# Optimization experiments

Measured on AMD Instinct MI355X. Metric: run time of the kernel, lower is better.

## Reference

```python
import jax, jax.numpy as jnp
import numpy as np

NH, NKV, HD = 32, 8, 64
ROPE_BASE = 10000.0


def _rope_tables(L, hd):
    inv_freq = 1.0 / (ROPE_BASE ** (jnp.arange(0, hd, 2, dtype=jnp.float32) / hd))
    t = jnp.arange(L, dtype=jnp.float32)
    freqs = jnp.outer(t, inv_freq)              # (L, hd/2)
    emb = jnp.concatenate([freqs, freqs], -1)   # (L, hd)
    return jnp.cos(emb), jnp.sin(emb)


def _rotate_half(x):
    h = x.shape[-1] // 2
    return jnp.concatenate([-x[..., h:], x[..., :h]], axis=-1)


def _apply_rope(x, cos, sin):
    # x: (B, H, L, hd); cos/sin: (L, hd) broadcast over B, H
    return x * cos[None, None] + _rotate_half(x) * sin[None, None]


def setup_inputs() -> dict:
    key = jax.random.key(0)
    ks = jax.random.split(key, 5)
    B, L, H = 2, 2048, 2048
    s = 0.02
    return {
        "x": jax.random.normal(ks[0], (B, L, H), dtype=jnp.float32),
        "wq": jax.random.normal(ks[1], (NH * HD, H), dtype=jnp.float32) * s,
        "wk": jax.random.normal(ks[2], (NKV * HD, H), dtype=jnp.float32) * s,
        "wv": jax.random.normal(ks[3], (NKV * HD, H), dtype=jnp.float32) * s,
        "wo": jax.random.normal(ks[4], (H, NH * HD), dtype=jnp.float32) * s,
    }


def reference(x, wq, wk, wv, wo):
    B, L, H = x.shape
    rep = NH // NKV
    q = (x @ wq.T).reshape(B, L, NH, HD).transpose(0, 2, 1, 3)    # (B, nh, L, hd)
    k = (x @ wk.T).reshape(B, L, NKV, HD).transpose(0, 2, 1, 3)   # (B, nkv, L, hd)
    v = (x @ wv.T).reshape(B, L, NKV, HD).transpose(0, 2, 1, 3)
    cos, sin = _rope_tables(L, HD)
    q = _apply_rope(q, cos, sin)
    k = _apply_rope(k, cos, sin)
    # GQA: group q heads instead of repeating K/V (same math as repeat_interleave)
    qg = q.reshape(B, NKV, rep, L, HD)
    scores = jnp.einsum("bgrqd,bgkd->bgrqk", qg, k) / jnp.sqrt(jnp.float32(HD))
    causal = jnp.tril(jnp.ones((L, L), dtype=bool))
    scores = jnp.where(causal, scores, jnp.float32(-jnp.inf))
    probs = jax.nn.softmax(scores, axis=-1)
    out = jnp.einsum("bgrqk,bgkd->bgrqd", probs, v)               # (B, nkv, rep, L, hd)
    out = out.reshape(B, NH, L, HD).transpose(0, 2, 1, 3).reshape(B, L, NH * HD)
    return out @ wo.T
```

## Files before the change

### kernel.cpp

```cpp
#include <hip/hip_runtime.h>

using u16 = unsigned short;
using u32 = unsigned int;
typedef __attribute__((ext_vector_type(8))) short bf16x8;
typedef __attribute__((ext_vector_type(4))) float f32x4;
typedef __attribute__((ext_vector_type(4))) float float4v;
typedef __attribute__((ext_vector_type(4))) unsigned short us4;
typedef __attribute__((ext_vector_type(2))) unsigned int u32x2;

__device__ __forceinline__ u16 f2bf(float f) {
  union { float f; unsigned u; } v; v.f = f;
  unsigned r = v.u + 0x7fffu + ((v.u >> 16) & 1u);
  return (u16)(r >> 16);
}

__device__ __forceinline__ u32 cvtpk(float a, float b) {
  u32 r;
  asm("v_cvt_pk_bf16_f32 %0, %1, %2" : "=v"(r) : "v"(a), "v"(b));
  return r;
}

__device__ __forceinline__ void glds16(const void* g, void* l) {
  __builtin_amdgcn_global_load_lds(
      (const __attribute__((address_space(1))) void*)g,
      (__attribute__((address_space(3))) void*)l, 16, 0, 0);
}

__device__ __forceinline__ void lgkm0() {
  asm volatile("s_waitcnt lgkmcnt(0)" ::: "memory");
}

#define MFMA(a, b, c) __builtin_amdgcn_mfma_f32_16x16x32_bf16((a), (b), (c), 0, 0, 0)

#define QSCALE 0.1803368801111601f

__global__ __launch_bounds__(256) void cvt_all(
    const float* __restrict__ x, const float* __restrict__ wq,
    const float* __restrict__ wk, const float* __restrict__ wv,
    const float* __restrict__ wo, u16* __restrict__ x_bf,
    u16* __restrict__ wqkv, u16* __restrict__ wo_bf) {
  int i = blockIdx.x * 256 + threadIdx.x;
  const float4v* src;
  us4* dst;
  if (i < 2097152) {
    src = (const float4v*)x + i; dst = (us4*)x_bf + i;
  } else if (i < 3145728) {
    int j = i - 2097152; src = (const float4v*)wq + j; dst = (us4*)wqkv + j;
  } else if (i < 3407872) {
    int j = i - 3145728; src = (const float4v*)wk + j; dst = (us4*)wqkv + 1048576 + j;
  } else if (i < 3670016) {
    int j = i - 3407872; src = (const float4v*)wv + j; dst = (us4*)wqkv + 1310720 + j;
  } else {
    int j = i - 3670016; src = (const float4v*)wo + j; dst = (us4*)wo_bf + j;
  }
  float4v v = *src;
  us4 o;
  o[0] = f2bf(v[0]); o[1] = f2bf(v[1]); o[2] = f2bf(v[2]); o[3] = f2bf(v[3]);
  *dst = o;
}

__global__ __launch_bounds__(256) void rope_cs(float2* __restrict__ cs) {
  int i = blockIdx.x * 256 + threadIdx.x;
  if (i >= 2048 * 32) return;
  int t = i >> 5, fi = i & 31;
  float inv = powf(10000.f, -(float)fi / 32.f);
  float ang = (float)t * inv;
  cs[i] = make_float2(cosf(ang), sinf(ang));
}

__global__ __launch_bounds__(256) void gemm_bt(const u16* __restrict__ A,
                                               const u16* __restrict__ B,
                                               float* __restrict__ C,
                                               int M, int N, int K) {
  __shared__ u16 As[128 * 32];
  __shared__ u16 Bs[128 * 32];
  const int nwg = gridDim.x;
  const int cpx = nwg >> 3;
  const int flat = blockIdx.x;
  const int swb = (flat & 7) * cpx + (flat >> 3);
  const int MT = M >> 7;
  const int bx = swb % MT, by = swb / MT;

  const int tid = threadIdx.x;
  const int w = tid >> 6, l = tid & 63;
  const int wr = w >> 1, wc = w & 1;
  const int lrow = l & 15, lk = (l >> 4) * 8, jr = (l >> 4) * 4;

  f32x4 acc[4][4];
#pragma unroll
  for (int m = 0; m < 4; ++m)
#pragma unroll
    for (int n = 0; n < 4; ++n) acc[m][n] = f32x4{0.f, 0.f, 0.f, 0.f};

  const int st_row = tid >> 2;
  const int st_k = (tid & 3) * 8;
  const u16* a0 = A + (size_t)(bx * 128 + st_row) * K + st_k;
  const u16* a1 = a0 + (size_t)64 * K;
  const u16* b0 = B + (size_t)(by * 128 + st_row) * K + st_k;
  const u16* b1 = b0 + (size_t)64 * K;

  u16* Ad0 = &As[w * 512];
  u16* Ad1 = &As[2048 + w * 512];
  u16* Bd0 = &Bs[w * 512];
  u16* Bd1 = &Bs[2048 + w * 512];

  for (int k0 = 0; k0 < K; k0 += 32) {
    glds16(a0, Ad0);
    glds16(a1, Ad1);
    glds16(b0, Bd0);
    glds16(b1, Bd1);
    a0 += 32; a1 += 32; b0 += 32; b1 += 32;
    __syncthreads();
    bf16x8 af[4], bfr[4];
#pragma unroll
    for (int m = 0; m < 4; ++m)
      af[m] = *(const bf16x8*)&As[(wr * 64 + m * 16 + lrow) * 32 + lk];
#pragma unroll
    for (int n = 0; n < 4; ++n)
      bfr[n] = *(const bf16x8*)&Bs[(wc * 64 + n * 16 + lrow) * 32 + lk];
#pragma unroll
    for (int m = 0; m < 4; ++m)
#pragma unroll
      for (int n = 0; n < 4; ++n)
        acc[m][n] = MFMA(af[m], bfr[n], acc[m][n]);
    __syncthreads();
  }

  float* Cp = C + (size_t)(bx * 128 + wr * 64) * N + by * 128 + wc * 64;
#pragma unroll
  for (int m = 0; m < 4; ++m)
#pragma unroll
    for (int n = 0; n < 4; ++n)
#pragma unroll
      for (int j = 0; j < 4; ++j)
        Cp[(size_t)(m * 16 + jr + j) * N + n * 16 + lrow] = acc[m][n][j];
}

__global__ __launch_bounds__(256) void gemm_qkv(const u16* __restrict__ A,
                                                const u16* __restrict__ B,
                                                const float2* __restrict__ cs,
                                                u16* __restrict__ q_r,
                                                u16* __restrict__ k_r,
                                                u16* __restrict__ v_t) {
  const int K = 2048;
  __shared__ u16 As[128 * 32];
  __shared__ u16 Bs[128 * 32];
  const int nwg = gridDim.x;
  const int cpx = nwg >> 3;
  const int flat = blockIdx.x;
  const int swb = (flat & 7) * cpx + (flat >> 3);
  const int bx = swb & 31, by = swb >> 5;

  const int tid = threadIdx.x;
  const int w = tid >> 6, l = tid & 63;
  const int wr = w >> 1, wc = w & 1;
  const int lrow = l & 15, lk = (l >> 4) * 8, jr = (l >> 4) * 4;

  f32x4 acc[4][4];
#pragma unroll
  for (int m = 0; m < 4; ++m)
#pragma unroll
    for (int n = 0; n < 4; ++n) acc[m][n] = f32x4{0.f, 0.f, 0.f, 0.f};

  const int st_row = tid >> 2;
  const int st_k = (tid & 3) * 8;
  const u16* a0 = A + (size_t)(bx * 128 + st_row) * K + st_k;
  const u16* a1 = a0 + (size_t)64 * K;
  const u16* b0 = B + (size_t)(by * 128 + st_row) * K + st_k;
  const u16* b1 = b0 + (size_t)64 * K;

  u16* Ad0 = &As[w * 512];
  u16* Ad1 = &As[2048 + w * 512];
  u16* Bd0 = &Bs[w * 512];
  u16* Bd1 = &Bs[2048 + w * 512];

  for (int k0 = 0; k0 < K; k0 += 32) {
    glds16(a0, Ad0);
    glds16(a1, Ad1);
    glds16(b0, Bd0);
    glds16(b1, Bd1);
    a0 += 32; a1 += 32; b0 += 32; b1 += 32;
    __syncthreads();
    bf16x8 af[4], bfr[4];
#pragma unroll
    for (int m = 0; m < 4; ++m)
      af[m] = *(const bf16x8*)&As[(wr * 64 + m * 16 + lrow) * 32 + lk];
#pragma unroll
    for (int n = 0; n < 4; ++n)
      bfr[n] = *(const bf16x8*)&Bs[(wc * 64 + n * 16 + lrow) * 32 + lk];
#pragma unroll
    for (int m = 0; m < 4; ++m)
#pragma unroll
      for (int n = 0; n < 4; ++n)
        acc[m][n] = MFMA(af[m], bfr[n], acc[m][n]);
    __syncthreads();
  }

  const int cb = by * 128 + wc * 64;
  const int rowbase = bx * 128 + wr * 64;

  if (cb < 2560) {
    const bool isQ = (cb < 2048);
    const int h = (isQ ? cb : cb - 2048) >> 6;
    u16* dst = isQ ? q_r : k_r;
    const int nh = isQ ? 32 : 8;
#pragma unroll
    for (int m = 0; m < 4; ++m) {
#pragma unroll
      for (int j = 0; j < 4; ++j) {
        const int row = rowbase + m * 16 + jr + j;
        const int b = row >> 11, ll = row & 2047;
        const float2 c0 = cs[ll * 32 + lrow];
        const float2 c1 = cs[ll * 32 + 16 + lrow];
        u16* op = dst + (((size_t)b * nh + h) * 2048 + ll) * 64;
#pragma unroll
        for (int n = 0; n < 4; ++n) {
          const float val = acc[m][n][j];
          const float oth = acc[m][n ^ 2][j];
          const float cx = (n & 1) ? c1.x : c0.x;
          const float sy = (n & 1) ? c1.y : c0.y;
          float r = (n < 2) ? (val * cx - oth * sy) : (val * cx + oth * sy);
          if (isQ) r *= QSCALE;
          op[n * 16 + lrow] = f2bf(r);
        }
      }
    }
  } else {
    const int h = (cb - 2560) >> 6;
#pragma unroll
    for (int m = 0; m < 4; ++m) {
      const int row0 = rowbase + m * 16 + jr;
      const int b = row0 >> 11, l0 = row0 & 2047;
#pragma unroll
      for (int n = 0; n < 4; ++n) {
        const int d = n * 16 + lrow;
        us4 pk;
#pragma unroll
        for (int j = 0; j < 4; ++j) pk[j] = f2bf(acc[m][n][j]);
        *(us4*)&v_t[(((size_t)b * 8 + h) * 64 + d) * 2048 + l0] = pk;
      }
    }
  }
}

__global__ __launch_bounds__(256) void attn4(const u16* __restrict__ q_r,
                                             const u16* __restrict__ k_r,
                                             const u16* __restrict__ v_t,
                                             u16* __restrict__ attn_o) {
  __shared__ u16 Kl[2][64 * 64];
  __shared__ u16 Vl[2][64 * 64];
  __shared__ u16 Pl[4][32 * 64];

  const int bid = blockIdx.x;
  const int q0 = (63 - (bid >> 4)) * 32;
  const int bk = bid & 15;
  const int b = bk >> 3, kvh = bk & 7;

  const int tid = threadIdx.x;
  const int w = tid >> 6;
  const int l = tid & 63;
  const int h = kvh * 4 + w;
  const int lr = l & 15, lg = l >> 4;

  const u16* Qp = q_r + (((size_t)(b * 32 + h)) * 2048 + q0) * 64;
  const u16* Kp = k_r + ((size_t)(b * 8 + kvh)) * 2048 * 64;
  const u16* Vp = v_t + ((size_t)(b * 8 + kvh)) * 64 * 2048;

  bf16x8 qf[2][2];
#pragma unroll
  for (int qh = 0; qh < 2; ++qh)
#pragma unroll
    for (int kh = 0; kh < 2; ++kh)
      qf[qh][kh] = *(const bf16x8*)&Qp[(qh * 16 + lr) * 64 + kh * 32 + lg * 8];

  bf16x8 ones;
#pragma unroll
  for (int i = 0; i < 8; ++i) ones[i] = (short)0x3F80;

  f32x4 o[2][4];
#pragma unroll
  for (int qh = 0; qh < 2; ++qh)
#pragma unroll
    for (int nf = 0; nf < 4; ++nf) o[qh][nf] = f32x4{0.f, 0.f, 0.f, 0.f};
  f32x4 lsv[2] = {f32x4{0.f, 0.f, 0.f, 0.f}, f32x4{0.f, 0.f, 0.f, 0.f}};

  const int sr = l >> 3;
  const int sc = (l & 7) ^ sr;
  const int nt = (q0 + 95) >> 6;
  const int nfull = q0 >> 6;

  auto stage = [&](int bufi, int t) {
#pragma unroll
    for (int p = 0; p < 2; ++p) {
      const int r = p * 32 + w * 8 + sr;
      glds16(Kp + (size_t)(t * 64 + r) * 64 + sc * 8, &Kl[bufi][(p * 32 + w * 8) * 64]);
      glds16(Vp + (size_t)r * 2048 + t * 64 + sc * 8, &Vl[bufi][(p * 32 + w * 8) * 64]);
    }
  };

  stage(0, 0);
  int buf = 0;
  for (int t = 0; t < nt; ++t) {
    __syncthreads();
    if (t + 1 < nt) stage(buf ^ 1, t + 1);
    const int kv0 = t * 64;

    f32x4 s[2][4];
#pragma unroll
    for (int qh = 0; qh < 2; ++qh)
#pragma unroll
      for (int kv4 = 0; kv4 < 4; ++kv4) s[qh][kv4] = f32x4{0.f, 0.f, 0.f, 0.f};
    const int swz = (lr & 7) << 4;
#pragma unroll
    for (int kv4 = 0; kv4 < 4; ++kv4) {
      const int kvr = kv4 * 16 + lr;
#pragma unroll
      for (int kh = 0; kh < 2; ++kh) {
        bf16x8 kf = *(const bf16x8*)((const char*)&Kl[buf][kvr * 64] +
                                     ((kh * 64 + lg * 16) ^ swz));
        s[0][kv4] = MFMA(kf, qf[0][kh], s[0][kv4]);
        s[1][kv4] = MFMA(kf, qf[1][kh], s[1][kv4]);
      }
    }

    const bool diag = (t >= nfull);
#pragma unroll
    for (int qh = 0; qh < 2; ++qh) {
      const int qrow = q0 + qh * 16 + lr;
      if (diag) {
#pragma unroll
        for (int kv4 = 0; kv4 < 4; ++kv4)
#pragma unroll
          for (int j = 0; j < 4; ++j)
            if ((kv0 + kv4 * 16 + lg * 4 + j) > qrow) s[qh][kv4][j] = -1e30f;
      }
#pragma unroll
      for (int kv4 = 0; kv4 < 4; ++kv4) {
        u32x2 pk;
        pk[0] = cvtpk(exp2f(s[qh][kv4][0]), exp2f(s[qh][kv4][1]));
        pk[1] = cvtpk(exp2f(s[qh][kv4][2]), exp2f(s[qh][kv4][3]));
        *(u32x2*)((char*)&Pl[w][(qh * 16 + lr) * 64] +
                  ((kv4 * 32 + lg * 8) ^ swz)) = pk;
      }
    }

    lgkm0();
#pragma unroll
    for (int k2 = 0; k2 < 2; ++k2) {
      bf16x8 pa[2];
#pragma unroll
      for (int qh = 0; qh < 2; ++qh)
        pa[qh] = *(const bf16x8*)((const char*)&Pl[w][(qh * 16 + lr) * 64] +
                                  ((k2 * 64 + lg * 16) ^ swz));
      lsv[0] = MFMA(pa[0], ones, lsv[0]);
      lsv[1] = MFMA(pa[1], ones, lsv[1]);
#pragma unroll
      for (int nf = 0; nf < 4; ++nf) {
        const int d = nf * 16 + lr;
        bf16x8 bv = *(const bf16x8*)((const char*)&Vl[buf][d * 64] +
                                     ((k2 * 64 + lg * 16) ^ swz));
        o[0][nf] = MFMA(pa[0], bv, o[0][nf]);
        o[1][nf] = MFMA(pa[1], bv, o[1][nf]);
      }
    }
    buf ^= 1;
  }

  u16* Op = attn_o + (size_t)b * 2048 * 2048 + h * 64;
#pragma unroll
  for (int qh = 0; qh < 2; ++qh) {
#pragma unroll
    for (int j = 0; j < 4; ++j) {
      const float inv = __builtin_amdgcn_rcpf(lsv[qh][j]);
      const int row = q0 + qh * 16 + lg * 4 + j;
#pragma unroll
      for (int nf = 0; nf < 4; ++nf)
        Op[(size_t)row * 2048 + nf * 16 + lr] = f2bf(o[qh][nf][j] * inv);
    }
  }
}

extern "C" void kernel_launch(void* const* d_in, const int* in_sizes, int n_in,
                              void* d_out, int out_size, void* d_ws, size_t ws_size,
                              hipStream_t stream) {
  const float* x = (const float*)d_in[0];
  const float* wq = (const float*)d_in[1];
  const float* wk = (const float*)d_in[2];
  const float* wv = (const float*)d_in[3];
  const float* wo = (const float*)d_in[4];
  float* out = (float*)d_out;

  char* p = (char*)d_ws;
  auto alloc = [&](size_t bytes) {
    char* r = p;
    p += (bytes + 255) & ~(size_t)255;
    return r;
  };
  u16* x_bf    = (u16*)alloc((size_t)8388608 * 2);
  u16* wqkv    = (u16*)alloc((size_t)3072 * 2048 * 2);
  u16* wo_bf   = (u16*)alloc((size_t)2048 * 2048 * 2);
  u16* q_r     = (u16*)alloc((size_t)8388608 * 2);
  u16* k_r     = (u16*)alloc((size_t)2097152 * 2);
  u16* v_t     = (u16*)alloc((size_t)2097152 * 2);
  u16* attn_o  = (u16*)alloc((size_t)8388608 * 2);
  float2* cs   = (float2*)alloc((size_t)65536 * 8);

  cvt_all<<<18432, 256, 0, stream>>>(x, wq, wk, wv, wo, x_bf, wqkv, wo_bf);
  rope_cs<<<256, 256, 0, stream>>>(cs);

  gemm_qkv<<<768, 256, 0, stream>>>(x_bf, wqkv, cs, q_r, k_r, v_t);

  attn4<<<1024, 256, 0, stream>>>(q_r, k_r, v_t, attn_o);

  gemm_bt<<<512, 256, 0, stream>>>(attn_o, wo_bf, out, 4096, 2048, 2048);
}
```

Before: 330.7 us.

## Triple-buffer LDS in GEMM kernels to overlap global loads with MFMA

Both the output-projection GEMM and the fused QKV GEMM now keep three LDS stages and prefetch two K-tiles ahead through global_load_lds. A single barrier per iteration waits on vmcnt(4), which replaces the two __syncthreads of the old load-sync-compute-sync loop. The goal is to hide global memory latency behind the MFMA work. In exchange the kernels use three times as much LDS (48KB per block), which may cut occupancy, and correctness depends on the hand-placed waitcnt and barrier ordering.

```diff
diff --git a/kernel.cpp b/kernel.cpp
--- a/kernel.cpp
+++ b/kernel.cpp
@@ -29,6 +29,12 @@
 __device__ __forceinline__ void lgkm0() {
   asm volatile("s_waitcnt lgkmcnt(0)" ::: "memory");
 }
+
+#define PIPE_BAR(N)                                        \
+  __builtin_amdgcn_sched_barrier(0);                       \
+  asm volatile("s_waitcnt vmcnt(" #N ")" ::: "memory");    \
+  __builtin_amdgcn_s_barrier();                            \
+  __builtin_amdgcn_sched_barrier(0);
 
 #define MFMA(a, b, c) __builtin_amdgcn_mfma_f32_16x16x32_bf16((a), (b), (c), 0, 0, 0)
 
@@ -72,8 +78,8 @@
                                                const u16* __restrict__ B,
                                                float* __restrict__ C,
                                                int M, int N, int K) {
-  __shared__ u16 As[128 * 32];
-  __shared__ u16 Bs[128 * 32];
+  __shared__ u16 As[3][128 * 32];
+  __shared__ u16 Bs[3][128 * 32];
   const int nwg = gridDim.x;
   const int cpx = nwg >> 3;
   const int flat = blockIdx.x;
@@ -99,32 +105,41 @@
   const u16* b0 = B + (size_t)(by * 128 + st_row) * K + st_k;
   const u16* b1 = b0 + (size_t)64 * K;
 
-  u16* Ad0 = &As[w * 512];
-  u16* Ad1 = &As[2048 + w * 512];
-  u16* Bd0 = &Bs[w * 512];
-  u16* Bd1 = &Bs[2048 + w * 512];
-
-  for (int k0 = 0; k0 < K; k0 += 32) {
-    glds16(a0, Ad0);
-    glds16(a1, Ad1);
-    glds16(b0, Bd0);
-    glds16(b1, Bd1);
-    a0 += 32; a1 += 32; b0 += 32; b1 += 32;
-    __syncthreads();
+  auto stage = [&](int t, int sb) {
+    const size_t ko = (size_t)t * 32;
+    glds16(a0 + ko, &As[sb][w * 512]);
+    glds16(a1 + ko, &As[sb][2048 + w * 512]);
+    glds16(b0 + ko, &Bs[sb][w * 512]);
+    glds16(b1 + ko, &Bs[sb][2048 + w * 512]);
+  };
+  auto compute = [&](int cb) {
     bf16x8 af[4], bfr[4];
 #pragma unroll
     for (int m = 0; m < 4; ++m)
-      af[m] = *(const bf16x8*)&As[(wr * 64 + m * 16 + lrow) * 32 + lk];
+      af[m] = *(const bf16x8*)&As[cb][(wr * 64 + m * 16 + lrow) * 32 + lk];
 #pragma unroll
     for (int n = 0; n < 4; ++n)
-      bfr[n] = *(const bf16x8*)&Bs[(wc * 64 + n * 16 + lrow) * 32 + lk];
+      bfr[n] = *(const bf16x8*)&Bs[cb][(wc * 64 + n * 16 + lrow) * 32 + lk];
 #pragma unroll
     for (int m = 0; m < 4; ++m)
 #pragma unroll
       for (int n = 0; n < 4; ++n)
         acc[m][n] = MFMA(af[m], bfr[n], acc[m][n]);
-    __syncthreads();
-  }
+  };
+
+  const int NT = K >> 5;
+  stage(0, 0);
+  stage(1, 1);
+  int cb = 0, sb = 2;
+  for (int t = 0; t < NT - 1; ++t) {
+    PIPE_BAR(4)
+    if (t + 2 < NT) stage(t + 2, sb);
+    compute(cb);
+    cb = (cb == 2) ? 0 : cb + 1;
+    sb = (sb == 2) ? 0 : sb + 1;
+  }
+  PIPE_BAR(0)
+  compute(cb);
 
   float* Cp = C + (size_t)(bx * 128 + wr * 64) * N + by * 128 + wc * 64;
 #pragma unroll
@@ -143,8 +158,8 @@
                                                 u16* __restrict__ k_r,
                                                 u16* __restrict__ v_t) {
   const int K = 2048;
-  __shared__ u16 As[128 * 32];
-  __shared__ u16 Bs[128 * 32];
+  __shared__ u16 As[3][128 * 32];
+  __shared__ u16 Bs[3][128 * 32];
   const int nwg = gridDim.x;
   const int cpx = nwg >> 3;
   const int flat = blockIdx.x;
@@ -169,39 +184,48 @@
   const u16* b0 = B + (size_t)(by * 128 + st_row) * K + st_k;
   const u16* b1 = b0 + (size_t)64 * K;
 
-  u16* Ad0 = &As[w * 512];
-  u16* Ad1 = &As[2048 + w * 512];
-  u16* Bd0 = &Bs[w * 512];
-  u16* Bd1 = &Bs[2048 + w * 512];
-
-  for (int k0 = 0; k0 < K; k0 += 32) {
-    glds16(a0, Ad0);
-    glds16(a1, Ad1);
-    glds16(b0, Bd0);
-    glds16(b1, Bd1);
-    a0 += 32; a1 += 32; b0 += 32; b1 += 32;
-    __syncthreads();
+  auto stage = [&](int t, int sbi) {
+    const size_t ko = (size_t)t * 32;
+    glds16(a0 + ko, &As[sbi][w * 512]);
+    glds16(a1 + ko, &As[sbi][2048 + w * 512]);
+    glds16(b0 + ko, &Bs[sbi][w * 512]);
+    glds16(b1 + ko, &Bs[sbi][2048 + w * 512]);
+  };
+  auto compute = [&](int cbi) {
     bf16x8 af[4], bfr[4];
 #pragma unroll
     for (int m = 0; m < 4; ++m)
-      af[m] = *(const bf16x8*)&As[(wr * 64 + m * 16 + lrow) * 32 + lk];
+      af[m] = *(const bf16x8*)&As[cbi][(wr * 64 + m * 16 + lrow) * 32 + lk];
 #pragma unroll
     for (int n = 0; n < 4; ++n)
-      bfr[n] = *(const bf16x8*)&Bs[(wc * 64 + n * 16 + lrow) * 32 + lk];
+      bfr[n] = *(const bf16x8*)&Bs[cbi][(wc * 64 + n * 16 + lrow) * 32 + lk];
 #pragma unroll
     for (int m = 0; m < 4; ++m)
 #pragma unroll
       for (int n = 0; n < 4; ++n)
         acc[m][n] = MFMA(af[m], bfr[n], acc[m][n]);
-    __syncthreads();
-  }
-
-  const int cb = by * 128 + wc * 64;
+  };
+
+  const int NT = K >> 5;
+  stage(0, 0);
+  stage(1, 1);
+  int cb = 0, sb = 2;
+  for (int t = 0; t < NT - 1; ++t) {
+    PIPE_BAR(4)
+    if (t + 2 < NT) stage(t + 2, sb);
+    compute(cb);
+    cb = (cb == 2) ? 0 : cb + 1;
+    sb = (sb == 2) ? 0 : sb + 1;
+  }
+  PIPE_BAR(0)
+  compute(cb);
+
+  const int cbcol = by * 128 + wc * 64;
   const int rowbase = bx * 128 + wr * 64;
 
-  if (cb < 2560) {
-    const bool isQ = (cb < 2048);
-    const int h = (isQ ? cb : cb - 2048) >> 6;
+  if (cbcol < 2560) {
+    const bool isQ = (cbcol < 2048);
+    const int h = (isQ ? cbcol : cbcol - 2048) >> 6;
     u16* dst = isQ ? q_r : k_r;
     const int nh = isQ ? 32 : 8;
 #pragma unroll
@@ -226,7 +250,7 @@
       }
     }
   } else {
-    const int h = (cb - 2560) >> 6;
+    const int h = (cbcol - 2560) >> 6;
 #pragma unroll
     for (int m = 0; m < 4; ++m) {
       const int row0 = rowbase + m * 16 + jr;
```

After: 345.1 us. 4.4% more time.

## Rewrite QKV and output GEMMs with larger tiles, double-buffered LDS and swizzle

Applied to the files above, without the earlier changes.

Replaces both projection GEMMs with 512-thread kernels that use larger block tiles (256x256 for QKV, 256x128 for the output projection) and a 64-wide K step. LDS is double-buffered, so the global-to-LDS load of the next tile overlaps compute on the current one, and an XOR swizzle avoids bank conflicts. MFMA phases are interleaved with barriers and priority raises. The goal is better operand reuse and fewer barriers per FLOP. In exchange the grids shrink to 192 and 256 workgroups, which may underfill the GPU's CUs, and the kernels use much more LDS.

```diff
diff --git a/kernel.cpp b/kernel.cpp
--- a/kernel.cpp
+++ b/kernel.cpp
@@ -29,6 +29,11 @@
 __device__ __forceinline__ void lgkm0() {
   asm volatile("s_waitcnt lgkmcnt(0)" ::: "memory");
 }
+
+#define TILE_GATE()                                      \
+  asm volatile("s_waitcnt vmcnt(0)" ::: "memory");       \
+  __builtin_amdgcn_s_barrier();                          \
+  __builtin_amdgcn_sched_barrier(0);
 
 #define MFMA(a, b, c) __builtin_amdgcn_mfma_f32_16x16x32_bf16((a), (b), (c), 0, 0, 0)
 
@@ -68,150 +73,148 @@
   cs[i] = make_float2(cosf(ang), sinf(ang));
 }
 
-__global__ __launch_bounds__(256) void gemm_bt(const u16* __restrict__ A,
-                                               const u16* __restrict__ B,
-                                               float* __restrict__ C,
-                                               int M, int N, int K) {
-  __shared__ u16 As[128 * 32];
-  __shared__ u16 Bs[128 * 32];
+__global__ __launch_bounds__(512, 2) void gemm_qkv(const u16* __restrict__ Ag,
+                                                   const u16* __restrict__ Bg,
+                                                   const float2* __restrict__ cs,
+                                                   u16* __restrict__ q_r,
+                                                   u16* __restrict__ k_r,
+                                                   u16* __restrict__ v_t) {
+  __shared__ u16 Al[2][256 * 64];
+  __shared__ u16 Bl[2][256 * 64];
+
   const int nwg = gridDim.x;
   const int cpx = nwg >> 3;
   const int flat = blockIdx.x;
   const int swb = (flat & 7) * cpx + (flat >> 3);
-  const int MT = M >> 7;
-  const int bx = swb % MT, by = swb / MT;
+  const int bx = swb & 15, by = swb >> 4;
+  const int bmRow = bx * 256, bnRow = by * 256;
 
   const int tid = threadIdx.x;
   const int w = tid >> 6, l = tid & 63;
-  const int wr = w >> 1, wc = w & 1;
-  const int lrow = l & 15, lk = (l >> 4) * 8, jr = (l >> 4) * 4;
-
-  f32x4 acc[4][4];
-#pragma unroll
-  for (int m = 0; m < 4; ++m)
+  const int wm = w >> 2, wn = w & 3;
+  const int lr = l & 15, lg = l >> 4;
+  const int rb7 = lr & 7;
+
+  const int srow = l >> 3;
+  const int sch = (l & 7) ^ srow;
+  const int reg0 = w * 32;
+  const u16* a_src = Ag + (size_t)(bmRow + reg0 + srow) * 2048 + sch * 8;
+  const u16* b_src = Bg + (size_t)(bnRow + reg0 + srow) * 2048 + sch * 8;
+
+  auto stageTile = [&](int kt, int bufi) {
+    const int kc = kt * 64;
+#pragma unroll
+    for (int i = 0; i < 4; ++i)
+      glds16(a_src + (size_t)i * 8 * 2048 + kc, &Al[bufi][(reg0 + i * 8) * 64]);
+#pragma unroll
+    for (int i = 0; i < 4; ++i)
+      glds16(b_src + (size_t)i * 8 * 2048 + kc, &Bl[bufi][(reg0 + i * 8) * 64]);
+  };
+  auto rd = [&](const u16* base, int row, int g) -> bf16x8 {
+    return *(const bf16x8*)((const char*)base + row * 128 + (((g) ^ rb7) << 4));
+  };
+
+  f32x4 acc[8][4];
+#pragma unroll
+  for (int m = 0; m < 8; ++m)
 #pragma unroll
     for (int n = 0; n < 4; ++n) acc[m][n] = f32x4{0.f, 0.f, 0.f, 0.f};
 
-  const int st_row = tid >> 2;
-  const int st_k = (tid & 3) * 8;
-  const u16* a0 = A + (size_t)(bx * 128 + st_row) * K + st_k;
-  const u16* a1 = a0 + (size_t)64 * K;
-  const u16* b0 = B + (size_t)(by * 128 + st_row) * K + st_k;
-  const u16* b1 = b0 + (size_t)64 * K;
-
-  u16* Ad0 = &As[w * 512];
-  u16* Ad1 = &As[2048 + w * 512];
-  u16* Bd0 = &Bs[w * 512];
-  u16* Bd1 = &Bs[2048 + w * 512];
-
-  for (int k0 = 0; k0 < K; k0 += 32) {
-    glds16(a0, Ad0);
-    glds16(a1, Ad1);
-    glds16(b0, Bd0);
-    glds16(b1, Bd1);
-    a0 += 32; a1 += 32; b0 += 32; b1 += 32;
-    __syncthreads();
-    bf16x8 af[4], bfr[4];
-#pragma unroll
-    for (int m = 0; m < 4; ++m)
-      af[m] = *(const bf16x8*)&As[(wr * 64 + m * 16 + lrow) * 32 + lk];
-#pragma unroll
-    for (int n = 0; n < 4; ++n)
-      bfr[n] = *(const bf16x8*)&Bs[(wc * 64 + n * 16 + lrow) * 32 + lk];
-#pragma unroll
-    for (int m = 0; m < 4; ++m)
-#pragma unroll
-      for (int n = 0; n < 4; ++n)
-        acc[m][n] = MFMA(af[m], bfr[n], acc[m][n]);
-    __syncthreads();
+  bf16x8 af[4][2], bfr[4][2];
+  const int NT = 32;
+
+  stageTile(0, 0);
+  for (int t = 0; t < NT; ++t) {
+    const int cur = t & 1;
+    const u16* Ab = &Al[cur][0];
+    const u16* Bb = &Bl[cur][0];
+
+    TILE_GATE()
+    if (t + 1 < NT) stageTile(t + 1, cur ^ 1);
+
+#pragma unroll
+    for (int m = 0; m < 4; ++m)
+#pragma unroll
+      for (int kk = 0; kk < 2; ++kk)
+        af[m][kk] = rd(Ab, wm * 128 + m * 16 + lr, kk * 4 + lg);
+#pragma unroll
+    for (int n = 0; n < 2; ++n)
+#pragma unroll
+      for (int kk = 0; kk < 2; ++kk)
+        bfr[n][kk] = rd(Bb, wn * 64 + n * 16 + lr, kk * 4 + lg);
+    __builtin_amdgcn_s_barrier();
+    __builtin_amdgcn_s_setprio(1);
+#pragma unroll
+    for (int m = 0; m < 4; ++m)
+#pragma unroll
+      for (int n = 0; n < 2; ++n)
+#pragma unroll
+        for (int kk = 0; kk < 2; ++kk)
+          acc[m][n] = MFMA(af[m][kk], bfr[n][kk], acc[m][n]);
+    __builtin_amdgcn_s_setprio(0);
+    __builtin_amdgcn_s_barrier();
+
+#pragma unroll
+    for (int n = 2; n < 4; ++n)
+#pragma unroll
+      for (int kk = 0; kk < 2; ++kk)
+        bfr[n][kk] = rd(Bb, wn * 64 + n * 16 + lr, kk * 4 + lg);
+    __builtin_amdgcn_s_barrier();
+    __builtin_amdgcn_s_setprio(1);
+#pragma unroll
+    for (int m = 0; m < 4; ++m)
+#pragma unroll
+      for (int n = 2; n < 4; ++n)
+#pragma unroll
+        for (int kk = 0; kk < 2; ++kk)
+          acc[m][n] = MFMA(af[m][kk], bfr[n][kk], acc[m][n]);
+    __builtin_amdgcn_s_setprio(0);
+    __builtin_amdgcn_s_barrier();
+
+#pragma unroll
+    for (int m = 0; m < 4; ++m)
+#pragma unroll
+      for (int kk = 0; kk < 2; ++kk)
+        af[m][kk] = rd(Ab, wm * 128 + 64 + m * 16 + lr, kk * 4 + lg);
+    __builtin_amdgcn_s_barrier();
+    __builtin_amdgcn_s_setprio(1);
+#pragma unroll
+    for (int m = 0; m < 4; ++m)
+#pragma unroll
+      for (int n = 0; n < 2; ++n)
+#pragma unroll
+        for (int kk = 0; kk < 2; ++kk)
+          acc[4 + m][n] = MFMA(af[m][kk], bfr[n][kk], acc[4 + m][n]);
+    __builtin_amdgcn_s_setprio(0);
+    __builtin_amdgcn_s_barrier();
+
+    __builtin_amdgcn_s_setprio(1);
+#pragma unroll
+    for (int m = 0; m < 4; ++m)
+#pragma unroll
+      for (int n = 2; n < 4; ++n)
+#pragma unroll
+        for (int kk = 0; kk < 2; ++kk)
+          acc[4 + m][n] = MFMA(af[m][kk], bfr[n][kk], acc[4 + m][n]);
+    __builtin_amdgcn_s_setprio(0);
   }
 
-  float* Cp = C + (size_t)(bx * 128 + wr * 64) * N + by * 128 + wc * 64;
-#pragma unroll
-  for (int m = 0; m < 4; ++m)
-#pragma unroll
-    for (int n = 0; n < 4; ++n)
-#pragma unroll
-      for (int j = 0; j < 4; ++j)
-        Cp[(size_t)(m * 16 + jr + j) * N + n * 16 + lrow] = acc[m][n][j];
-}
-
-__global__ __launch_bounds__(256) void gemm_qkv(const u16* __restrict__ A,
-                                                const u16* __restrict__ B,
-                                                const float2* __restrict__ cs,
-                                                u16* __restrict__ q_r,
-                                                u16* __restrict__ k_r,
-                                                u16* __restrict__ v_t) {
-  const int K = 2048;
-  __shared__ u16 As[128 * 32];
-  __shared__ u16 Bs[128 * 32];
-  const int nwg = gridDim.x;
-  const int cpx = nwg >> 3;
-  const int flat = blockIdx.x;
-  const int swb = (flat & 7) * cpx + (flat >> 3);
-  const int bx = swb & 31, by = swb >> 5;
-
-  const int tid = threadIdx.x;
-  const int w = tid >> 6, l = tid & 63;
-  const int wr = w >> 1, wc = w & 1;
-  const int lrow = l & 15, lk = (l >> 4) * 8, jr = (l >> 4) * 4;
-
-  f32x4 acc[4][4];
-#pragma unroll
-  for (int m = 0; m < 4; ++m)
-#pragma unroll
-    for (int n = 0; n < 4; ++n) acc[m][n] = f32x4{0.f, 0.f, 0.f, 0.f};
-
-  const int st_row = tid >> 2;
-  const int st_k = (tid & 3) * 8;
-  const u16* a0 = A + (size_t)(bx * 128 + st_row) * K + st_k;
-  const u16* a1 = a0 + (size_t)64 * K;
-  const u16* b0 = B + (size_t)(by * 128 + st_row) * K + st_k;
-  const u16* b1 = b0 + (size_t)64 * K;
-
-  u16* Ad0 = &As[w * 512];
-  u16* Ad1 = &As[2048 + w * 512];
-  u16* Bd0 = &Bs[w * 512];
-  u16* Bd1 = &Bs[2048 + w * 512];
-
-  for (int k0 = 0; k0 < K; k0 += 32) {
-    glds16(a0, Ad0);
-    glds16(a1, Ad1);
-    glds16(b0, Bd0);
-    glds16(b1, Bd1);
-    a0 += 32; a1 += 32; b0 += 32; b1 += 32;
-    __syncthreads();
-    bf16x8 af[4], bfr[4];
-#pragma unroll
-    for (int m = 0; m < 4; ++m)
-      af[m] = *(const bf16x8*)&As[(wr * 64 + m * 16 + lrow) * 32 + lk];
-#pragma unroll
-    for (int n = 0; n < 4; ++n)
-      bfr[n] = *(const bf16x8*)&Bs[(wc * 64 + n * 16 + lrow) * 32 + lk];
-#pragma unroll
-    for (int m = 0; m < 4; ++m)
-#pragma unroll
-      for (int n = 0; n < 4; ++n)
-        acc[m][n] = MFMA(af[m], bfr[n], acc[m][n]);
-    __syncthreads();
-  }
-
-  const int cb = by * 128 + wc * 64;
-  const int rowbase = bx * 128 + wr * 64;
-
-  if (cb < 2560) {
-    const bool isQ = (cb < 2048);
-    const int h = (isQ ? cb : cb - 2048) >> 6;
+  const int cbcol = bnRow + wn * 64;
+  const int rowbase = bmRow + wm * 128;
+
+  if (cbcol < 2560) {
+    const bool isQ = (cbcol < 2048);
+    const int h = (isQ ? cbcol : cbcol - 2048) >> 6;
     u16* dst = isQ ? q_r : k_r;
     const int nh = isQ ? 32 : 8;
 #pragma unroll
-    for (int m = 0; m < 4; ++m) {
+    for (int m = 0; m < 8; ++m) {
 #pragma unroll
       for (int j = 0; j < 4; ++j) {
-        const int row = rowbase + m * 16 + jr + j;
+        const int row = rowbase + m * 16 + lg * 4 + j;
         const int b = row >> 11, ll = row & 2047;
-        const float2 c0 = cs[ll * 32 + lrow];
-        const float2 c1 = cs[ll * 32 + 16 + lrow];
+        const float2 c0 = cs[ll * 32 + lr];
+        const float2 c1 = cs[ll * 32 + 16 + lr];
         u16* op = dst + (((size_t)b * nh + h) * 2048 + ll) * 64;
 #pragma unroll
         for (int n = 0; n < 4; ++n) {
@@ -221,19 +224,19 @@
           const float sy = (n & 1) ? c1.y : c0.y;
           float r = (n < 2) ? (val * cx - oth * sy) : (val * cx + oth * sy);
           if (isQ) r *= QSCALE;
-          op[n * 16 + lrow] = f2bf(r);
+          op[n * 16 + lr] = f2bf(r);
         }
       }
     }
   } else {
-    const int h = (cb - 2560) >> 6;
-#pragma unroll
-    for (int m = 0; m < 4; ++m) {
-      const int row0 = rowbase + m * 16 + jr;
+    const int h = (cbcol - 2560) >> 6;
+#pragma unroll
+    for (int m = 0; m < 8; ++m) {
+      const int row0 = rowbase + m * 16 + lg * 4;
       const int b = row0 >> 11, l0 = row0 & 2047;
 #pragma unroll
       for (int n = 0; n < 4; ++n) {
-        const int d = n * 16 + lrow;
+        const int d = n * 16 + lr;
         us4 pk;
 #pragma unroll
         for (int j = 0; j < 4; ++j) pk[j] = f2bf(acc[m][n][j]);
@@ -241,6 +244,112 @@
       }
     }
   }
+}
+
+__global__ __launch_bounds__(512, 2) void gemm_o(const u16* __restrict__ Ag,
+                                                 const u16* __restrict__ Bg,
+                                                 float* __restrict__ C) {
+  __shared__ u16 Al[2][256 * 64];
+  __shared__ u16 Bl[2][128 * 64];
+
+  const int nwg = gridDim.x;
+  const int cpx = nwg >> 3;
+  const int flat = blockIdx.x;
+  const int swb = (flat & 7) * cpx + (flat >> 3);
+  const int bx = swb & 15, by = swb >> 4;
+  const int bmRow = bx * 256, bnRow = by * 128;
+
+  const int tid = threadIdx.x;
+  const int w = tid >> 6, l = tid & 63;
+  const int wm = w >> 1, wn = w & 1;
+  const int lr = l & 15, lg = l >> 4;
+  const int rb7 = lr & 7;
+
+  const int srow = l >> 3;
+  const int sch = (l & 7) ^ srow;
+  const int areg = w * 32;
+  const int breg = w * 16;
+  const u16* a_src = Ag + (size_t)(bmRow + areg + srow) * 2048 + sch * 8;
+  const u16* b_src = Bg + (size_t)(bnRow + breg + srow) * 2048 + sch * 8;
+
+  auto stageTile = [&](int kt, int bufi) {
+    const int kc = kt * 64;
+#pragma unroll
+    for (int i = 0; i < 4; ++i)
+      glds16(a_src + (size_t)i * 8 * 2048 + kc, &Al[bufi][(areg + i * 8) * 64]);
+#pragma unroll
+    for (int i = 0; i < 2; ++i)
+      glds16(b_src + (size_t)i * 8 * 2048 + kc, &Bl[bufi][(breg + i * 8) * 64]);
+  };
+  auto rd = [&](const u16* base, int row, int g) -> bf16x8 {
+    return *(const bf16x8*)((const char*)base + row * 128 + (((g) ^ rb7) << 4));
+  };
+
+  f32x4 acc[4][4];
+#pragma unroll
+  for (int m = 0; m < 4; ++m)
+#pragma unroll
+    for (int n = 0; n < 4; ++n) acc[m][n] = f32x4{0.f, 0.f, 0.f, 0.f};
+
+  bf16x8 af[4][2], bfr[4][2];
+  const int NT = 32;
+
+  stageTile(0, 0);
+  for (int t = 0; t < NT; ++t) {
+    const int cur = t & 1;
+    const u16* Ab = &Al[cur][0];
+    const u16* Bb = &Bl[cur][0];
+
+    TILE_GATE()
+    if (t + 1 < NT) stageTile(t + 1, cur ^ 1);
+
+#pragma unroll
+    for (int m = 0; m < 4; ++m)
+#pragma unroll
+      for (int kk = 0; kk < 2; ++kk)
+        af[m][kk] = rd(Ab, wm * 64 + m * 16 + lr, kk * 4 + lg);
+#pragma unroll
+    for (int n = 0; n < 2; ++n)
+#pragma unroll
+      for (int kk = 0; kk < 2; ++kk)
+        bfr[n][kk] = rd(Bb, wn * 64 + n * 16 + lr, kk * 4 + lg);
+    __builtin_amdgcn_s_barrier();
+    __builtin_amdgcn_s_setprio(1);
+#pragma unroll
+    for (int m = 0; m < 4; ++m)
+#pragma unroll
+      for (int n = 0; n < 2; ++n)
+#pragma unroll
+        for (int kk = 0; kk < 2; ++kk)
+          acc[m][n] = MFMA(af[m][kk], bfr[n][kk], acc[m][n]);
+    __builtin_amdgcn_s_setprio(0);
+    __builtin_amdgcn_s_barrier();
+
+#pragma unroll
+    for (int n = 2; n < 4; ++n)
+#pragma unroll
+      for (int kk = 0; kk < 2; ++kk)
+        bfr[n][kk] = rd(Bb, wn * 64 + n * 16 + lr, kk * 4 + lg);
+    __builtin_amdgcn_s_barrier();
+    __builtin_amdgcn_s_setprio(1);
+#pragma unroll
+    for (int m = 0; m < 4; ++m)
+#pragma unroll
+      for (int n = 2; n < 4; ++n)
+#pragma unroll
+        for (int kk = 0; kk < 2; ++kk)
+          acc[m][n] = MFMA(af[m][kk], bfr[n][kk], acc[m][n]);
+    __builtin_amdgcn_s_setprio(0);
+  }
+
+  float* Cp = C + (size_t)(bmRow + wm * 64) * 2048 + bnRow + wn * 64;
+#pragma unroll
+  for (int m = 0; m < 4; ++m)
+#pragma unroll
+    for (int n = 0; n < 4; ++n)
+#pragma unroll
+      for (int j = 0; j < 4; ++j)
+        Cp[(size_t)(m * 16 + lg * 4 + j) * 2048 + n * 16 + lr] = acc[m][n][j];
 }
 
 __global__ __launch_bounds__(256) void attn4(const u16* __restrict__ q_r,
@@ -408,9 +517,9 @@
   cvt_all<<<18432, 256, 0, stream>>>(x, wq, wk, wv, wo, x_bf, wqkv, wo_bf);
   rope_cs<<<256, 256, 0, stream>>>(cs);
 
-  gemm_qkv<<<768, 256, 0, stream>>>(x_bf, wqkv, cs, q_r, k_r, v_t);
+  gemm_qkv<<<192, 512, 0, stream>>>(x_bf, wqkv, cs, q_r, k_r, v_t);
 
   attn4<<<1024, 256, 0, stream>>>(q_r, k_r, v_t, attn_o);
 
-  gemm_bt<<<512, 256, 0, stream>>>(attn_o, wo_bf, out, 4096, 2048, 2048);
-}
+  gemm_o<<<256, 512, 0, stream>>>(attn_o, wo_bf, out);
+}
```

After: 318.2 us. -3.8%, faster.
